# Performance work log

Measured on AMD Instinct MI355X. Metric: run time of the kernel, lower is better.

## Reference

```python
import jax, jax.numpy as jnp
import numpy as np

TOP_K = 2

def setup_inputs() -> dict:
    key = jax.random.key(0)
    k1, k2, k3, k4 = jax.random.split(key, 4)
    T, H, I, E = 8192, 2048, 4096, 8
    s = 0.02
    return {
        "hidden_states": jax.random.normal(k1, (T, H), dtype=jnp.float32),
        "router_w": jax.random.normal(k2, (E, H), dtype=jnp.float32) * s,
        "ws": jax.random.normal(k3, (E, 2 * I, H), dtype=jnp.float32) * s,  # [gate; up]
        "w2s": jax.random.normal(k4, (E, H, I), dtype=jnp.float32) * s,
    }

def reference(hidden_states, router_w, ws, w2s):
    # Router gating: softmax over experts, top-k, NO renormalization
    logits = hidden_states @ router_w.T              # [T, E]
    probs = jax.nn.softmax(logits, axis=-1)
    topv, topi = jax.lax.top_k(probs, TOP_K)         # [T, K]
    T, E = probs.shape
    I = w2s.shape[2]
    # Dense routing-weight matrix [T, E]; top_k indices are unique per token
    w = jnp.zeros_like(probs).at[jnp.arange(T)[:, None], topi].set(topv)
    out = jnp.zeros_like(hidden_states)
    for e in range(E):  # fixed small expert loop; avoids [T,E,2I] blowup
        gate = hidden_states @ ws[e, :I].T           # [T, I]
        up = hidden_states @ ws[e, I:].T             # [T, I]
        h = jax.nn.silu(gate) * up                   # SwiGLU
        out = out + w[:, e:e + 1] * (h @ w2s[e].T)   # combine
    return out
```

## Files before the change

### kernel.cpp

```cpp
#include <hip/hip_runtime.h>
#include <cstdint>
#include <cstddef>

#define T_TOK 8192
#define HDIM  2048
#define IDIM  4096
#define NEXP  8
#define MAXT  72

typedef __bf16 bf16x8 __attribute__((ext_vector_type(8)));
typedef float  f32x4  __attribute__((ext_vector_type(4)));

#define BARRIER() __builtin_amdgcn_s_barrier()
#define LGKM0()   do { asm volatile("s_waitcnt lgkmcnt(0)" ::: "memory"); __builtin_amdgcn_sched_barrier(0); } while (0)
#define VMW(n)    do { asm volatile("s_waitcnt vmcnt(" #n ")" ::: "memory"); } while (0)
#define PRIO1()   __builtin_amdgcn_s_setprio(1)
#define PRIO0()   __builtin_amdgcn_s_setprio(0)

__device__ __forceinline__ unsigned short f2bf(float f) {
    union { float f; unsigned u; } v; v.f = f;
    unsigned r = v.u + 0x7FFFu + ((v.u >> 16) & 1u);
    return (unsigned short)(r >> 16);
}

__device__ __forceinline__ void gload16(const void* g, void* l) {
    __builtin_amdgcn_global_load_lds((__attribute__((address_space(1))) void*)g,
                                     (__attribute__((address_space(3))) void*)l,
                                     16, 0, 0);
}

__global__ __launch_bounds__(256) void router_k(const float* __restrict__ hs,
                                                const float* __restrict__ rw,
                                                float* __restrict__ wgt,
                                                int* __restrict__ counts,
                                                int* __restrict__ lists) {
    int gid  = blockIdx.x * 256 + threadIdx.x;
    int tok  = gid >> 6;
    int lane = threadIdx.x & 63;
    const float* x = hs + (size_t)tok * HDIM;

    float acc[NEXP];
#pragma unroll
    for (int e = 0; e < NEXP; ++e) acc[e] = 0.f;
    for (int h = lane; h < HDIM; h += 64) {
        float xv = x[h];
#pragma unroll
        for (int e = 0; e < NEXP; ++e) acc[e] = fmaf(xv, rw[e * HDIM + h], acc[e]);
    }
#pragma unroll
    for (int off = 32; off > 0; off >>= 1) {
#pragma unroll
        for (int e = 0; e < NEXP; ++e) acc[e] += __shfl_xor(acc[e], off, 64);
    }
    if (lane == 0) {
        float m = acc[0];
#pragma unroll
        for (int e = 1; e < NEXP; ++e) m = fmaxf(m, acc[e]);
        float p[NEXP]; float s = 0.f;
#pragma unroll
        for (int e = 0; e < NEXP; ++e) { p[e] = expf(acc[e] - m); s += p[e]; }
        float inv = 1.f / s;
        int i1 = 0;
#pragma unroll
        for (int e = 1; e < NEXP; ++e) if (acc[e] > acc[i1]) i1 = e;
        int i2 = -1;
#pragma unroll
        for (int e = 0; e < NEXP; ++e) if (e != i1 && (i2 < 0 || acc[e] > acc[i2])) i2 = e;
#pragma unroll
        for (int e = 0; e < NEXP; ++e)
            wgt[(size_t)tok * NEXP + e] = (e == i1 || e == i2) ? p[e] * inv : 0.f;
        int p1 = atomicAdd(&counts[i1], 1);
        lists[i1 * T_TOK + p1] = tok;
        int p2 = atomicAdd(&counts[i2], 1);
        lists[i2 * T_TOK + p2] = (1 << 16) | tok;
    }
}

__global__ void plan_k(const int* __restrict__ counts, int* __restrict__ offs,
                       int* __restrict__ desc, int* __restrict__ ntiles) {
    if (threadIdx.x == 0 && blockIdx.x == 0) {
        int off = 0, n = 0;
        for (int e = 0; e < NEXP; ++e) {
            offs[e] = off;
            int nt = (counts[e] + 255) >> 8;
            for (int t = 0; t < nt; ++t) desc[n++] = (e << 16) | t;
            off += nt * 256;
        }
        *ntiles = n;
    }
}

__global__ __launch_bounds__(256) void cvt_k(const float* __restrict__ in,
                                             unsigned short* __restrict__ out, long n4) {
    long i      = (long)blockIdx.x * 256 + threadIdx.x;
    long stride = (long)gridDim.x * 256;
    const float4* in4 = (const float4*)in;
    ushort4* out4 = (ushort4*)out;
    for (long j = i; j < n4; j += stride) {
        float4 v = in4[j];
        ushort4 o;
        o.x = f2bf(v.x); o.y = f2bf(v.y); o.z = f2bf(v.z); o.w = f2bf(v.w);
        out4[j] = o;
    }
}

__global__ __launch_bounds__(512, 2) void gemm1_k(const unsigned short* __restrict__ A,
                                                  const unsigned short* __restrict__ Wall,
                                                  unsigned short* __restrict__ Hout,
                                                  const int* __restrict__ lists,
                                                  const int* __restrict__ counts,
                                                  const int* __restrict__ offs,
                                                  const int* __restrict__ desc,
                                                  const int* __restrict__ ntiles) {
    const int slot = blockIdx.y;
    if (slot >= *ntiles) return;
    const int dsc = desc[slot];
    const int e = dsc >> 16, tt = dsc & 0xFFFF;
    const int cnt = counts[e];
    const int t0 = tt * 256;
    const int* list = lists + e * T_TOK;
    const unsigned short* W = Wall + (size_t)e * 2 * IDIM * HDIM;
    const int hbase = offs[e];
    const int n0 = blockIdx.x * 128;

    extern __shared__ __align__(16) char lds[];

    const int tid  = threadIdx.x;
    const int lane = tid & 63;
    const int wid  = tid >> 6;
    const int wr   = wid >> 2;
    const int wc   = wid & 3;

    const int prow = tid >> 3;
    const int pcol = (tid & 7) * 16;
    const int lcol = (pcol ^ ((prow & 7) << 4)) >> 1;
    unsigned aoff[4];
#pragma unroll
    for (int i = 0; i < 4; ++i) {
        int g = t0 + i * 64 + prow;
        int tok = list[(g < cnt) ? g : t0] & 0xFFFF;
        aoff[i] = (unsigned)tok * HDIM + lcol;
    }
    unsigned goff[2], uoff[2];
#pragma unroll
    for (int i = 0; i < 2; ++i) {
        goff[i] = (unsigned)(n0 + i * 64 + prow) * HDIM + lcol;
        uoff[i] = (unsigned)(IDIM + n0 + i * 64 + prow) * HDIM + lcol;
    }
    const int dst = tid * 16;

#define G1_STAGE(buf, kt) do {                                                     \
    unsigned k0_ = (unsigned)(kt) * 64;                                            \
    _Pragma("unroll") for (int i_ = 0; i_ < 4; ++i_)                               \
        gload16(A + aoff[i_] + k0_, lds + (buf) * 32768 + i_ * 8192 + dst);        \
    _Pragma("unroll") for (int i_ = 0; i_ < 2; ++i_)                               \
        gload16(W + goff[i_] + k0_, lds + 65536 + (buf) * 16384 + i_ * 8192 + dst);\
    _Pragma("unroll") for (int i_ = 0; i_ < 2; ++i_)                               \
        gload16(W + uoff[i_] + k0_, lds + 98304 + (buf) * 16384 + i_ * 8192 + dst);\
} while (0)

    const int frd = (lane & 7) << 4;
    const int cb0 = (((lane >> 4) * 16)     ) ^ frd;
    const int cb1 = (((lane >> 4) * 16) | 64) ^ frd;
    const int arow = wr * 16384 + (lane & 15) * 128;
    const int brow = (wc * 32 + (lane & 15)) * 128;

    f32x4 accg[8][2], accu[8][2];
#pragma unroll
    for (int mi = 0; mi < 8; ++mi)
#pragma unroll
        for (int ni = 0; ni < 2; ++ni) {
            accg[mi][ni] = (f32x4){0.f, 0.f, 0.f, 0.f};
            accu[mi][ni] = (f32x4){0.f, 0.f, 0.f, 0.f};
        }

    G1_STAGE(0, 0);
    G1_STAGE(1, 1);
    VMW(8);
    BARRIER();

    const int NT = HDIM / 64;
    int buf = 0;
    for (int kt = 0; kt < NT; ++kt) {
        const char* la = lds + buf * 32768 + arow;
        const char* lg = lds + 65536 + buf * 16384 + brow;
        const char* lu = lds + 98304 + buf * 16384 + brow;
        bf16x8 af[4], bg[2], bu[2];
#pragma unroll
        for (int mi = 0; mi < 4; ++mi) af[mi] = *(const bf16x8*)(la + mi * 2048 + cb0);
#pragma unroll
        for (int ni = 0; ni < 2; ++ni) {
            bg[ni] = *(const bf16x8*)(lg + ni * 2048 + cb0);
            bu[ni] = *(const bf16x8*)(lu + ni * 2048 + cb0);
        }
        LGKM0(); PRIO1();
#pragma unroll
        for (int mi = 0; mi < 4; ++mi)
#pragma unroll
            for (int ni = 0; ni < 2; ++ni) {
                accg[mi][ni] = __builtin_amdgcn_mfma_f32_16x16x32_bf16(af[mi], bg[ni], accg[mi][ni], 0, 0, 0);
                accu[mi][ni] = __builtin_amdgcn_mfma_f32_16x16x32_bf16(af[mi], bu[ni], accu[mi][ni], 0, 0, 0);
            }
        PRIO0();
#pragma unroll
        for (int mi = 0; mi < 4; ++mi) af[mi] = *(const bf16x8*)(la + (mi + 4) * 2048 + cb0);
        LGKM0(); PRIO1();
#pragma unroll
        for (int mi = 0; mi < 4; ++mi)
#pragma unroll
            for (int ni = 0; ni < 2; ++ni) {
                accg[mi + 4][ni] = __builtin_amdgcn_mfma_f32_16x16x32_bf16(af[mi], bg[ni], accg[mi + 4][ni], 0, 0, 0);
                accu[mi + 4][ni] = __builtin_amdgcn_mfma_f32_16x16x32_bf16(af[mi], bu[ni], accu[mi + 4][ni], 0, 0, 0);
            }
        PRIO0();
#pragma unroll
        for (int mi = 0; mi < 4; ++mi) af[mi] = *(const bf16x8*)(la + mi * 2048 + cb1);
#pragma unroll
        for (int ni = 0; ni < 2; ++ni) {
            bg[ni] = *(const bf16x8*)(lg + ni * 2048 + cb1);
            bu[ni] = *(const bf16x8*)(lu + ni * 2048 + cb1);
        }
        LGKM0(); PRIO1();
#pragma unroll
        for (int mi = 0; mi < 4; ++mi)
#pragma unroll
            for (int ni = 0; ni < 2; ++ni) {
                accg[mi][ni] = __builtin_amdgcn_mfma_f32_16x16x32_bf16(af[mi], bg[ni], accg[mi][ni], 0, 0, 0);
                accu[mi][ni] = __builtin_amdgcn_mfma_f32_16x16x32_bf16(af[mi], bu[ni], accu[mi][ni], 0, 0, 0);
            }
        PRIO0();
#pragma unroll
        for (int mi = 0; mi < 4; ++mi) af[mi] = *(const bf16x8*)(la + (mi + 4) * 2048 + cb1);
        LGKM0();
        BARRIER();
        G1_STAGE(buf, (kt + 2) & (NT - 1));
        PRIO1();
#pragma unroll
        for (int mi = 0; mi < 4; ++mi)
#pragma unroll
            for (int ni = 0; ni < 2; ++ni) {
                accg[mi + 4][ni] = __builtin_amdgcn_mfma_f32_16x16x32_bf16(af[mi], bg[ni], accg[mi + 4][ni], 0, 0, 0);
                accu[mi + 4][ni] = __builtin_amdgcn_mfma_f32_16x16x32_bf16(af[mi], bu[ni], accu[mi + 4][ni], 0, 0, 0);
            }
        PRIO0();
        VMW(8);
        BARRIER();
        buf ^= 1;
    }
    VMW(0);
#undef G1_STAGE

#pragma unroll
    for (int mi = 0; mi < 8; ++mi)
#pragma unroll
        for (int ni = 0; ni < 2; ++ni)
#pragma unroll
            for (int j = 0; j < 4; ++j) {
                int row = hbase + t0 + wr * 128 + mi * 16 + ((lane >> 4) << 2) + j;
                int col = n0 + wc * 32 + ni * 16 + (lane & 15);
                float g = accg[mi][ni][j], u = accu[mi][ni][j];
                float hv = (g / (1.f + expf(-g))) * u;
                Hout[(size_t)row * IDIM + col] = f2bf(hv);
            }
}

__global__ __launch_bounds__(512, 2) void gemm2_k(const unsigned short* __restrict__ Ah,
                                                  const unsigned short* __restrict__ Ball,
                                                  const float* __restrict__ wgt,
                                                  float* __restrict__ outP,
                                                  const int* __restrict__ lists,
                                                  const int* __restrict__ counts,
                                                  const int* __restrict__ offs,
                                                  const int* __restrict__ desc,
                                                  const int* __restrict__ ntiles) {
    const int slot = blockIdx.y;
    if (slot >= *ntiles) return;
    const int dsc = desc[slot];
    const int e = dsc >> 16, tt = dsc & 0xFFFF;
    const int cnt = counts[e];
    const int t0 = tt * 256;
    const int* list = lists + e * T_TOK;
    const unsigned short* B = Ball + (size_t)e * HDIM * IDIM;
    const int hbase = offs[e];
    const int n0 = blockIdx.x * 256;

    extern __shared__ __align__(16) char lds[];

    const int tid  = threadIdx.x;
    const int lane = tid & 63;
    const int wid  = tid >> 6;
    const int wr   = wid >> 2;
    const int wc   = wid & 3;

    const int prow = tid >> 3;
    const int pcol = (tid & 7) * 16;
    const int lcol = (pcol ^ ((prow & 7) << 4)) >> 1;
    unsigned aoff[4], boff[4];
#pragma unroll
    for (int i = 0; i < 4; ++i) {
        aoff[i] = (unsigned)(hbase + t0 + i * 64 + prow) * IDIM + lcol;
        boff[i] = (unsigned)(n0 + i * 64 + prow) * IDIM + lcol;
    }
    const int dst = tid * 16;

#define G2_STAGE(buf, kt) do {                                                     \
    unsigned k0_ = (unsigned)(kt) * 64;                                            \
    _Pragma("unroll") for (int i_ = 0; i_ < 4; ++i_)                               \
        gload16(Ah + aoff[i_] + k0_, lds + (buf) * 32768 + i_ * 8192 + dst);       \
    _Pragma("unroll") for (int i_ = 0; i_ < 4; ++i_)                               \
        gload16(B + boff[i_] + k0_, lds + 65536 + (buf) * 32768 + i_ * 8192 + dst);\
} while (0)

    const int frd = (lane & 7) << 4;
    const int cb0 = (((lane >> 4) * 16)     ) ^ frd;
    const int cb1 = (((lane >> 4) * 16) | 64) ^ frd;
    const int arow = wr * 16384 + (lane & 15) * 128;
    const int brow = (wc * 64 + (lane & 15)) * 128;

    f32x4 acc[8][4];
#pragma unroll
    for (int mi = 0; mi < 8; ++mi)
#pragma unroll
        for (int ni = 0; ni < 4; ++ni) acc[mi][ni] = (f32x4){0.f, 0.f, 0.f, 0.f};

    G2_STAGE(0, 0);
    G2_STAGE(1, 1);
    VMW(8);
    BARRIER();

    const int NT = IDIM / 64;
    int buf = 0;
    for (int kt = 0; kt < NT; ++kt) {
        const char* la = lds + buf * 32768 + arow;
        const char* lb = lds + 65536 + buf * 32768 + brow;
        bf16x8 af[4], bfr[4];
#pragma unroll
        for (int mi = 0; mi < 4; ++mi) af[mi] = *(const bf16x8*)(la + mi * 2048 + cb0);
#pragma unroll
        for (int ni = 0; ni < 4; ++ni) bfr[ni] = *(const bf16x8*)(lb + ni * 2048 + cb0);
        LGKM0(); PRIO1();
#pragma unroll
        for (int mi = 0; mi < 4; ++mi)
#pragma unroll
            for (int ni = 0; ni < 4; ++ni)
                acc[mi][ni] = __builtin_amdgcn_mfma_f32_16x16x32_bf16(af[mi], bfr[ni], acc[mi][ni], 0, 0, 0);
        PRIO0();
#pragma unroll
        for (int mi = 0; mi < 4; ++mi) af[mi] = *(const bf16x8*)(la + (mi + 4) * 2048 + cb0);
        LGKM0(); PRIO1();
#pragma unroll
        for (int mi = 0; mi < 4; ++mi)
#pragma unroll
            for (int ni = 0; ni < 4; ++ni)
                acc[mi + 4][ni] = __builtin_amdgcn_mfma_f32_16x16x32_bf16(af[mi], bfr[ni], acc[mi + 4][ni], 0, 0, 0);
        PRIO0();
#pragma unroll
        for (int mi = 0; mi < 4; ++mi) af[mi] = *(const bf16x8*)(la + mi * 2048 + cb1);
#pragma unroll
        for (int ni = 0; ni < 4; ++ni) bfr[ni] = *(const bf16x8*)(lb + ni * 2048 + cb1);
        LGKM0(); PRIO1();
#pragma unroll
        for (int mi = 0; mi < 4; ++mi)
#pragma unroll
            for (int ni = 0; ni < 4; ++ni)
                acc[mi][ni] = __builtin_amdgcn_mfma_f32_16x16x32_bf16(af[mi], bfr[ni], acc[mi][ni], 0, 0, 0);
        PRIO0();
#pragma unroll
        for (int mi = 0; mi < 4; ++mi) af[mi] = *(const bf16x8*)(la + (mi + 4) * 2048 + cb1);
        LGKM0();
        BARRIER();
        G2_STAGE(buf, (kt + 2) & (NT - 1));
        PRIO1();
#pragma unroll
        for (int mi = 0; mi < 4; ++mi)
#pragma unroll
            for (int ni = 0; ni < 4; ++ni)
                acc[mi + 4][ni] = __builtin_amdgcn_mfma_f32_16x16x32_bf16(af[mi], bfr[ni], acc[mi + 4][ni], 0, 0, 0);
        PRIO0();
        VMW(8);
        BARRIER();
        buf ^= 1;
    }
    VMW(0);
#undef G2_STAGE

#pragma unroll
    for (int mi = 0; mi < 8; ++mi)
#pragma unroll
        for (int j = 0; j < 4; ++j) {
            int g = t0 + wr * 128 + mi * 16 + ((lane >> 4) << 2) + j;
            if (g < cnt) {
                int ent = list[g];
                int tok = ent & 0xFFFF;
                int sl  = ent >> 16;
                float w = wgt[(size_t)tok * NEXP + e];
                float* o = outP + (size_t)sl * T_TOK * HDIM + (size_t)tok * HDIM;
#pragma unroll
                for (int ni = 0; ni < 4; ++ni) {
                    int col = n0 + wc * 64 + ni * 16 + (lane & 15);
                    o[col] = w * acc[mi][ni][j];
                }
            }
        }
}

__global__ __launch_bounds__(256) void combine_k(const float* __restrict__ p0,
                                                 const float* __restrict__ p1,
                                                 float* __restrict__ out, long n4) {
    long i      = (long)blockIdx.x * 256 + threadIdx.x;
    long stride = (long)gridDim.x * 256;
    const float4* a4 = (const float4*)p0;
    const float4* b4 = (const float4*)p1;
    float4* o4 = (float4*)out;
    for (long j = i; j < n4; j += stride) {
        float4 a = a4[j], b = b4[j];
        o4[j] = make_float4(a.x + b.x, a.y + b.y, a.z + b.z, a.w + b.w);
    }
}

extern "C" void kernel_launch(void* const* d_in, const int* in_sizes, int n_in,
                              void* d_out, int out_size, void* d_ws, size_t ws_size,
                              hipStream_t stream) {
    const float* hs  = (const float*)d_in[0];
    const float* rw  = (const float*)d_in[1];
    const float* ws  = (const float*)d_in[2];
    const float* w2s = (const float*)d_in[3];
    float* out = (float*)d_out;

    char* wsp = (char*)d_ws;
    unsigned short* hs_bf = (unsigned short*)(wsp);
    unsigned short* w_bf  = (unsigned short*)(wsp + 33554432ULL);
    unsigned short* w2_bf = (unsigned short*)(wsp + 301989888ULL);
    unsigned short* h_bf  = (unsigned short*)(wsp + 436207616ULL);
    float*          outP  = (float*)(wsp + 587202560ULL);
    float*          wgt   = (float*)(wsp + 721420288ULL);
    int*            counts = (int*)(wsp + 721682432ULL);
    int*            offs   = (int*)(wsp + 721682560ULL);
    int*            lists  = (int*)(wsp + 721682688ULL);
    int*            desc   = (int*)(wsp + 721944832ULL);
    int*            ntiles = (int*)(wsp + 721945344ULL);

    hipMemsetAsync(counts, 0, NEXP * sizeof(int), stream);
    cvt_k<<<2048, 256, 0, stream>>>(hs, hs_bf, (long)T_TOK * HDIM / 4);
    cvt_k<<<4096, 256, 0, stream>>>(ws, w_bf, (long)NEXP * 2 * IDIM * HDIM / 4);
    cvt_k<<<4096, 256, 0, stream>>>(w2s, w2_bf, (long)NEXP * HDIM * IDIM / 4);
    router_k<<<(T_TOK * 64) / 256, 256, 0, stream>>>(hs, rw, wgt, counts, lists);
    plan_k<<<1, 64, 0, stream>>>(counts, offs, desc, ntiles);

    gemm1_k<<<dim3(IDIM / 128, MAXT), 512, 131072, stream>>>(
        hs_bf, w_bf, h_bf, lists, counts, offs, desc, ntiles);
    gemm2_k<<<dim3(HDIM / 256, MAXT), 512, 131072, stream>>>(
        h_bf, w2_bf, wgt, outP, lists, counts, offs, desc, ntiles);
    combine_k<<<2048, 256, 0, stream>>>(outP, outP + (size_t)T_TOK * HDIM, out,
                                        (long)T_TOK * HDIM / 4);
}
```

Baseline: 1.494 ms.

## Shrink gemm2 tile to 256x128 with K=32 stages for higher occupancy

Reworks the second grouped GEMM from a 256x256 tile with K-step 64 and 128 KB of dynamic LDS to a 256x128 tile with K-step 32 and 48 KB of static LDS. Each wave now owns a 64x64 subtile, and launch bounds ask for 4 blocks per CU. The goal is more resident blocks and twice as many blocks in the grid, to better hide latency and fill the GPU. The cost is lower arithmetic intensity per tile, twice as many K iterations each with two barriers, and more global traffic for the A operand.

```diff
diff --git a/kernel.cpp b/kernel.cpp
--- a/kernel.cpp
+++ b/kernel.cpp
@@ -264,7 +264,7 @@
             }
 }
 
-__global__ __launch_bounds__(512, 2) void gemm2_k(const unsigned short* __restrict__ Ah,
+__global__ __launch_bounds__(512, 4) void gemm2_k(const unsigned short* __restrict__ Ah,
                                                   const unsigned short* __restrict__ Ball,
                                                   const float* __restrict__ wgt,
                                                   float* __restrict__ outP,
@@ -282,102 +282,73 @@
     const int* list = lists + e * T_TOK;
     const unsigned short* B = Ball + (size_t)e * HDIM * IDIM;
     const int hbase = offs[e];
-    const int n0 = blockIdx.x * 256;
-
-    extern __shared__ __align__(16) char lds[];
+    const int n0 = blockIdx.x * 128;
+
+    __shared__ __align__(16) char lds[49152];
 
     const int tid  = threadIdx.x;
     const int lane = tid & 63;
     const int wid  = tid >> 6;
-    const int wr   = wid >> 2;
-    const int wc   = wid & 3;
-
-    const int prow = tid >> 3;
-    const int pcol = (tid & 7) * 16;
-    const int lcol = (pcol ^ ((prow & 7) << 4)) >> 1;
-    unsigned aoff[4], boff[4];
-#pragma unroll
-    for (int i = 0; i < 4; ++i) {
-        aoff[i] = (unsigned)(hbase + t0 + i * 64 + prow) * IDIM + lcol;
-        boff[i] = (unsigned)(n0 + i * 64 + prow) * IDIM + lcol;
-    }
+    const int wr   = wid >> 1;
+    const int wc   = wid & 1;
+
+    const int prow = tid >> 2;
+    const int pcol = (tid & 3) * 16;
+    const int lcol = (pcol ^ (((prow >> 1) & 3) << 4)) >> 1;
+    const unsigned aoff0 = (unsigned)(hbase + t0 + prow) * IDIM + lcol;
+    const unsigned aoff1 = (unsigned)(hbase + t0 + 128 + prow) * IDIM + lcol;
+    const unsigned boff  = (unsigned)(n0 + prow) * IDIM + lcol;
     const int dst = tid * 16;
 
-#define G2_STAGE(buf, kt) do {                                                     \
-    unsigned k0_ = (unsigned)(kt) * 64;                                            \
-    _Pragma("unroll") for (int i_ = 0; i_ < 4; ++i_)                               \
-        gload16(Ah + aoff[i_] + k0_, lds + (buf) * 32768 + i_ * 8192 + dst);       \
-    _Pragma("unroll") for (int i_ = 0; i_ < 4; ++i_)                               \
-        gload16(B + boff[i_] + k0_, lds + 65536 + (buf) * 32768 + i_ * 8192 + dst);\
+#define G2_STAGE(buf, kt) do {                                        \
+    unsigned k0_ = (unsigned)(kt) * 32;                               \
+    gload16(Ah + aoff0 + k0_, lds + (buf) * 16384 + dst);             \
+    gload16(Ah + aoff1 + k0_, lds + (buf) * 16384 + 8192 + dst);      \
+    gload16(B + boff + k0_, lds + 32768 + (buf) * 8192 + dst);        \
 } while (0)
 
-    const int frd = (lane & 7) << 4;
-    const int cb0 = (((lane >> 4) * 16)     ) ^ frd;
-    const int cb1 = (((lane >> 4) * 16) | 64) ^ frd;
-    const int arow = wr * 16384 + (lane & 15) * 128;
-    const int brow = (wc * 64 + (lane & 15)) * 128;
-
-    f32x4 acc[8][4];
-#pragma unroll
-    for (int mi = 0; mi < 8; ++mi)
+    const int cb = ((lane >> 4) << 4) ^ (((lane >> 1) & 3) << 4);
+    const int arow = wr * 4096 + (lane & 15) * 64;
+    const int brow = wc * 4096 + (lane & 15) * 64;
+
+    f32x4 acc[4][4];
+#pragma unroll
+    for (int mi = 0; mi < 4; ++mi)
 #pragma unroll
         for (int ni = 0; ni < 4; ++ni) acc[mi][ni] = (f32x4){0.f, 0.f, 0.f, 0.f};
 
     G2_STAGE(0, 0);
     G2_STAGE(1, 1);
-    VMW(8);
+    VMW(3);
     BARRIER();
 
-    const int NT = IDIM / 64;
+    const int NT = IDIM / 32;
     int buf = 0;
     for (int kt = 0; kt < NT; ++kt) {
-        const char* la = lds + buf * 32768 + arow;
-        const char* lb = lds + 65536 + buf * 32768 + brow;
+        const char* la = lds + buf * 16384 + arow;
+        const char* lb = lds + 32768 + buf * 8192 + brow;
         bf16x8 af[4], bfr[4];
 #pragma unroll
-        for (int mi = 0; mi < 4; ++mi) af[mi] = *(const bf16x8*)(la + mi * 2048 + cb0);
-#pragma unroll
-        for (int ni = 0; ni < 4; ++ni) bfr[ni] = *(const bf16x8*)(lb + ni * 2048 + cb0);
+        for (int mi = 0; mi < 4; ++mi) af[mi] = *(const bf16x8*)(la + mi * 1024 + cb);
+#pragma unroll
+        for (int ni = 0; ni < 4; ++ni) bfr[ni] = *(const bf16x8*)(lb + ni * 1024 + cb);
         LGKM0(); PRIO1();
 #pragma unroll
         for (int mi = 0; mi < 4; ++mi)
 #pragma unroll
-            for (int ni = 0; ni < 4; ++ni)
+            for (int ni = 0; ni < 2; ++ni)
                 acc[mi][ni] = __builtin_amdgcn_mfma_f32_16x16x32_bf16(af[mi], bfr[ni], acc[mi][ni], 0, 0, 0);
         PRIO0();
-#pragma unroll
-        for (int mi = 0; mi < 4; ++mi) af[mi] = *(const bf16x8*)(la + (mi + 4) * 2048 + cb0);
-        LGKM0(); PRIO1();
-#pragma unroll
-        for (int mi = 0; mi < 4; ++mi)
-#pragma unroll
-            for (int ni = 0; ni < 4; ++ni)
-                acc[mi + 4][ni] = __builtin_amdgcn_mfma_f32_16x16x32_bf16(af[mi], bfr[ni], acc[mi + 4][ni], 0, 0, 0);
-        PRIO0();
-#pragma unroll
-        for (int mi = 0; mi < 4; ++mi) af[mi] = *(const bf16x8*)(la + mi * 2048 + cb1);
-#pragma unroll
-        for (int ni = 0; ni < 4; ++ni) bfr[ni] = *(const bf16x8*)(lb + ni * 2048 + cb1);
-        LGKM0(); PRIO1();
-#pragma unroll
-        for (int mi = 0; mi < 4; ++mi)
-#pragma unroll
-            for (int ni = 0; ni < 4; ++ni)
-                acc[mi][ni] = __builtin_amdgcn_mfma_f32_16x16x32_bf16(af[mi], bfr[ni], acc[mi][ni], 0, 0, 0);
-        PRIO0();
-#pragma unroll
-        for (int mi = 0; mi < 4; ++mi) af[mi] = *(const bf16x8*)(la + (mi + 4) * 2048 + cb1);
-        LGKM0();
         BARRIER();
         G2_STAGE(buf, (kt + 2) & (NT - 1));
         PRIO1();
 #pragma unroll
         for (int mi = 0; mi < 4; ++mi)
 #pragma unroll
-            for (int ni = 0; ni < 4; ++ni)
-                acc[mi + 4][ni] = __builtin_amdgcn_mfma_f32_16x16x32_bf16(af[mi], bfr[ni], acc[mi + 4][ni], 0, 0, 0);
-        PRIO0();
-        VMW(8);
+            for (int ni = 2; ni < 4; ++ni)
+                acc[mi][ni] = __builtin_amdgcn_mfma_f32_16x16x32_bf16(af[mi], bfr[ni], acc[mi][ni], 0, 0, 0);
+        PRIO0();
+        VMW(3);
         BARRIER();
         buf ^= 1;
     }
@@ -385,10 +356,10 @@
 #undef G2_STAGE
 
 #pragma unroll
-    for (int mi = 0; mi < 8; ++mi)
+    for (int mi = 0; mi < 4; ++mi)
 #pragma unroll
         for (int j = 0; j < 4; ++j) {
-            int g = t0 + wr * 128 + mi * 16 + ((lane >> 4) << 2) + j;
+            int g = t0 + wr * 64 + mi * 16 + ((lane >> 4) << 2) + j;
             if (g < cnt) {
                 int ent = list[g];
                 int tok = ent & 0xFFFF;
@@ -449,7 +420,7 @@
 
     gemm1_k<<<dim3(IDIM / 128, MAXT), 512, 131072, stream>>>(
         hs_bf, w_bf, h_bf, lists, counts, offs, desc, ntiles);
-    gemm2_k<<<dim3(HDIM / 256, MAXT), 512, 131072, stream>>>(
+    gemm2_k<<<dim3(HDIM / 128, MAXT), 512, 0, stream>>>(
         h_bf, w2_bf, wgt, outP, lists, counts, offs, desc, ntiles);
     combine_k<<<2048, 256, 0, stream>>>(outP, outP + (size_t)T_TOK * HDIM, out,
                                         (long)T_TOK * HDIM / 4);
```

Result: faster. 1.455 ms (-2.6%).
